# Performance work log

Measured on AMD Instinct MI355X. Metric: run time of the kernel, lower is better.

## Reference

```python
import jax, jax.numpy as jnp
import numpy as np

B, C, H, W = 4, 256, 64, 64
CQK = C // 16  # 16


def conv2d(x, w, b):
    # x: [B,C,H,W], w: [O,I,3,3], SAME padding, stride 1
    y = jax.lax.conv_general_dilated(
        x, w, window_strides=(1, 1), padding='SAME',
        dimension_numbers=('NCHW', 'OIHW', 'NCHW'))
    return y + b[None, :, None, None]


def setup_inputs() -> dict:
    key = jax.random.key(0)
    ks = jax.random.split(key, 8)
    fan_in = C * 9
    s = 1.0 / np.sqrt(fan_in)
    return {
        'x': jax.random.normal(ks[0], (B, C, H, W), jnp.float32),
        'y': jax.random.normal(ks[1], (B, C, H, W), jnp.float32),
        'wq': jax.random.normal(ks[2], (CQK, C, 3, 3), jnp.float32) * s,
        'bq': jnp.zeros((CQK,), jnp.float32),
        'wk': jax.random.normal(ks[3], (CQK, C, 3, 3), jnp.float32) * s,
        'bk': jnp.zeros((CQK,), jnp.float32),
        'wv': jax.random.normal(ks[4], (C, C, 3, 3), jnp.float32) * s,
        'bv': jnp.zeros((C,), jnp.float32),
    }


def reference(x, y, wq, bq, wk, bk, wv, bv):
    b, c, h, w = x.shape
    n = h * w
    q = conv2d(x, wq, bq).reshape(b, -1, n)            # [B,CQK,N]
    k = conv2d(y, wk, bk).reshape(b, -1, n)            # [B,CQK,N]
    v = conv2d(y, wv, bv).reshape(b, c, n)             # [B,C,N]
    # energy[b,i,j] = sum_d q[b,d,i] * k[b,d,j]  (unscaled, as in source)
    energy = jnp.einsum('bdi,bdj->bij', q, k)          # [B,N,N]
    attn = jax.nn.softmax(energy, axis=-1)
    # out[b,c,i] = sum_j v[b,c,j] * attn[b,i,j]
    out = jnp.einsum('bcj,bij->bci', v, attn)
    return out.reshape(b, c, h, w)
```

## Files before the change

### kernel.cpp

```cpp
#include <hip/hip_runtime.h>
#include <stdint.h>


typedef __bf16 bf16;
typedef bf16 bf16x8 __attribute__((ext_vector_type(8)));
typedef float f32x4 __attribute__((ext_vector_type(4)));
typedef unsigned long long ull;

#define DEV static __device__ __forceinline__

DEV f32x4 mfma16(bf16x8 a, bf16x8 b, f32x4 c) {
  return __builtin_amdgcn_mfma_f32_16x16x32_bf16(a, b, c, 0, 0, 0);
}

#define SMBUF 25344
#define YSLAB 4224

__global__ void pack_all_kernel(const float* __restrict__ wv, const float* __restrict__ wq,
                                const float* __restrict__ wk, bf16* __restrict__ W3v,
                                bf16* __restrict__ W3q, bf16* __restrict__ W3k) {
  int idx = blockIdx.x * 256 + threadIdx.x;
  if (idx >= 663552) return;
  const float* src;
  bf16* dst;
  int rel, O;
  if (idx < 589824)      { src = wv; dst = W3v; rel = idx; O = 256; }
  else if (idx < 626688) { src = wq; dst = W3q; rel = idx - 589824; O = 16; }
  else                   { src = wk; dst = W3k; rel = idx - 626688; O = 16; }
  int o = rel / 2304, r = rel - o * 2304;
  int ci = r / 9, tap = r - ci * 9;
  int chunk = ci >> 6, c6 = ci & 63;
  int ks = (tap << 1) + (c6 >> 5), j = c6 & 31;
  dst[((chunk * 18 + ks) * O + o) * 32 + j] = (bf16)src[rel];
}

DEV void stage_load(float4* xv, const float* __restrict__ img, int b, int h, int ci0, int t) {
  const int wg = t & 15, clq = t >> 4;
#pragma unroll
  for (int dh = 0; dh < 3; ++dh) {
    int hh = h + dh - 1;
    bool ok = (hh >= 0) && (hh < 64);
#pragma unroll
    for (int cc = 0; cc < 4; ++cc) {
      float4 v = make_float4(0.f, 0.f, 0.f, 0.f);
      if (ok) v = *(const float4*)&img[((((size_t)b << 8) + ci0 + (clq << 2) + cc) * 64 + hh) * 64 + (wg << 2)];
      xv[dh * 4 + cc] = v;
    }
  }
}

DEV void stage_write(char* smc, const float4* xv, int t) {
  if (t < 96) {
    int dh = t >> 5, r = t & 31;
    int wH = (r & 16) ? 65 : 0, cq = r & 15;
    *(ull*)(smc + ((((dh * 66 + wH) << 7) + (cq << 3)) ^ ((wH & 7) << 4))) = 0ull;
  }
  const int wg = t & 15, clq = t >> 4;
#pragma unroll
  for (int dh = 0; dh < 3; ++dh) {
    const float4 a = xv[dh * 4 + 0], b4 = xv[dh * 4 + 1], c4 = xv[dh * 4 + 2], d4 = xv[dh * 4 + 3];
    const float ax[4] = {a.x, a.y, a.z, a.w};
    const float bx[4] = {b4.x, b4.y, b4.z, b4.w};
    const float cx[4] = {c4.x, c4.y, c4.z, c4.w};
    const float dx[4] = {d4.x, d4.y, d4.z, d4.w};
#pragma unroll
    for (int q4 = 0; q4 < 4; ++q4) {
      int wH = (wg << 2) + q4 + 1;
      union { bf16 h4[4]; ull v; } pk;
      pk.h4[0] = (bf16)ax[q4]; pk.h4[1] = (bf16)bx[q4];
      pk.h4[2] = (bf16)cx[q4]; pk.h4[3] = (bf16)dx[q4];
      *(ull*)(smc + ((((dh * 66 + wH) << 7) + (clq << 3)) ^ ((wH & 7) << 4))) = pk.v;
    }
  }
}

DEV void yF_write(bf16* __restrict__ yFo, const float4* xv, int b, int h, int chunk, int t) {
  const int wg = t & 15, clq = t >> 4;
  const int half = clq >> 3, gr = clq & 7;
  ull* base = (ull*)yFo + ((size_t)(((b * 64 + h) * 4 + chunk) * 2 + half) * 66) * 8 + gr;
  const float4 a = xv[4 + 0], b4 = xv[4 + 1], c4 = xv[4 + 2], d4 = xv[4 + 3];
  const float ax[4] = {a.x, a.y, a.z, a.w};
  const float bx[4] = {b4.x, b4.y, b4.z, b4.w};
  const float cx[4] = {c4.x, c4.y, c4.z, c4.w};
  const float dx[4] = {d4.x, d4.y, d4.z, d4.w};
#pragma unroll
  for (int q4 = 0; q4 < 4; ++q4) {
    int wH = (wg << 2) + q4 + 1;
    union { bf16 h4[4]; ull v; } pk;
    pk.h4[0] = (bf16)ax[q4]; pk.h4[1] = (bf16)bx[q4];
    pk.h4[2] = (bf16)cx[q4]; pk.h4[3] = (bf16)dx[q4];
    base[(size_t)wH * 8] = pk.v;
  }
}

__global__ __launch_bounds__(256) void conv_qk_kernel(
    const float* __restrict__ x, const float* __restrict__ y,
    const bf16* __restrict__ W3q, const bf16* __restrict__ W3k,
    const float* __restrict__ bq, const float* __restrict__ bk,
    bf16* __restrict__ qT, bf16* __restrict__ kT, bf16* __restrict__ yFo) {
  __shared__ __align__(16) char smc[2 * SMBUF];
  const int mode = blockIdx.x >> 8;
  const float* img = mode ? y : x;
  const bf16* W3 = mode ? W3k : W3q;
  const float* bias = mode ? bk : bq;
  const int bi = blockIdx.x & 255;
  const int t = threadIdx.x;
  const int lane = t & 63, wv = t >> 6;
  const int g = lane >> 4, ln = lane & 15;
  const int b = bi >> 6;
  const int h = bi & 63;
  f32x4 acc = {0.f, 0.f, 0.f, 0.f};
  float4 xv[12];
  stage_load(xv, img, b, h, 0, t);
  if (mode) {
    if (t < 128) {
      int chunk = t >> 5, half = (t >> 4) & 1, wside = (t >> 3) & 1, gr = t & 7;
      int wH = wside ? 65 : 0;
      ((ull*)yFo)[((size_t)(((b * 64 + h) * 4 + chunk) * 2 + half) * 66 + wH) * 8 + gr] = 0ull;
    }
    yF_write(yFo, xv, b, h, 0, t);
  }
  stage_write(smc, xv, t);
  __syncthreads();
  for (int chunk = 0; chunk < 4; ++chunk) {
    char* cur = smc + (chunk & 1) * SMBUF;
    if (chunk < 3) {
      stage_load(xv, img, b, h, (chunk + 1) << 6, t);
      if (mode) yF_write(yFo, xv, b, h, chunk + 1, t);
    }
#pragma unroll
    for (int ks = 0; ks < 18; ++ks) {
      const int tap = ks >> 1, clb = (ks & 1) << 5;
      const int kh = tap / 3, kw = tap - kh * 3;
      const int wH = (wv << 4) + ln + kw;
      uint32_t bo = ((((kh * 66 + wH) << 6) + clb + (g << 3)) << 1) ^ ((wH & 7) << 4);
      bf16x8 bfr = *(const bf16x8*)(cur + bo);
      bf16x8 afr = *(const bf16x8*)&W3[(size_t)((chunk * 18 + ks) * 16 + ln) * 32 + (g << 3)];
      acc = mfma16(afr, bfr, acc);
    }
    if (chunk < 3) stage_write(smc + ((chunk + 1) & 1) * SMBUF, xv, t);
    __syncthreads();
  }
  const int p = (h << 6) + (wv << 4) + ln;
#pragma unroll
  for (int r = 0; r < 4; ++r) {
    int o = (g << 2) + r;
    float val = acc[r] + bias[o];
    if (mode == 0) {
      val *= 1.4426950408889634f;
      bf16* drow = qT + (((size_t)b << 12) + p) * 64;
      bf16 hi = (bf16)val;
      drow[o] = hi;
      drow[16 + o] = hi;
      drow[32 + o] = (bf16)(val - (float)hi);
      drow[48 + o] = (bf16)0.f;
    } else {
      bf16* drow = kT + (((size_t)b << 12) + p) * 32;
      bf16 hi = (bf16)val;
      drow[o] = hi;
      drow[16 + o] = (bf16)(val - (float)hi);
    }
  }
}

__global__ __launch_bounds__(256) void conv_v_kernel(
    const bf16* __restrict__ yF, const bf16* __restrict__ W3,
    const float* __restrict__ bias, bf16* __restrict__ VF) {
  __shared__ __align__(16) char smc[6 * YSLAB];
  const int t = threadIdx.x;
  const int lane = t & 63, wv = t >> 6;
  const int g = lane >> 4, ln = lane & 15;
  const int raw = blockIdx.x;
  const int b = raw >> 8;
  const int h = (raw >> 2) & 63;
  const int oh = raw & 3;
  const int obase = (oh << 6) + (wv << 4);
  const int kh0 = (h == 0) ? 1 : 0, kh1 = (h == 63) ? 2 : 3;
  f32x4 acc[4];
#pragma unroll
  for (int wf = 0; wf < 4; ++wf) acc[wf] = (f32x4){0.f, 0.f, 0.f, 0.f};

  f32x4 xmain[6];
  f32x4 xtail[6];
#define YBASE(kh, half, chunk) ((const char*)yF + \
    (size_t)((((b * 64 + (h + (kh) - 1)) * 4 + (chunk)) * 2 + (half)) * YSLAB))

#define LOADC(chunk)                                                       \
  {                                                                        \
    _Pragma("unroll")                                                      \
    for (int kh = 0; kh < 3; ++kh)                                         \
      if (kh >= kh0 && kh < kh1)                                           \
        _Pragma("unroll")                                                  \
        for (int half = 0; half < 2; ++half) {                             \
          const char* src = YBASE(kh, half, chunk);                        \
          xmain[kh * 2 + half] = *(const f32x4*)(src + (t << 4));          \
          if (t < 8) xtail[kh * 2 + half] = *(const f32x4*)(src + 4096 + (t << 4)); \
        }                                                                  \
  }

#define WRITEC()                                                           \
  {                                                                        \
    _Pragma("unroll")                                                      \
    for (int kh = 0; kh < 3; ++kh)                                         \
      if (kh >= kh0 && kh < kh1)                                           \
        _Pragma("unroll")                                                  \
        for (int half = 0; half < 2; ++half) {                             \
          char* dst = smc + (kh * 2 + half) * YSLAB;                       \
          *(f32x4*)(dst + (t << 4)) = xmain[kh * 2 + half];                \
          if (t < 8) *(f32x4*)(dst + 4096 + (t << 4)) = xtail[kh * 2 + half]; \
        }                                                                  \
  }

  LOADC(0)
  WRITEC()
  __syncthreads();
  for (int chunk = 0; chunk < 4; ++chunk) {
    if (chunk < 3) LOADC(chunk + 1)
#pragma unroll
    for (int kh = 0; kh < 3; ++kh) {
      if (kh < kh0 || kh >= kh1) continue;
      bf16x8 afr[6];
#pragma unroll
      for (int i = 0; i < 6; ++i) {
        const int ks = kh * 6 + i;
        afr[i] = *(const bf16x8*)&W3[(size_t)((chunk * 18 + ks) * 256 + obase + ln) * 32 + (g << 3)];
      }
#pragma unroll
      for (int i = 0; i < 6; ++i) {
        const int kw = i >> 1, half = i & 1;
        const char* lrow = smc + (kh * 2 + half) * YSLAB + ((ln + kw) << 6) + (g << 4);
#pragma unroll
        for (int wf = 0; wf < 4; ++wf) {
          bf16x8 bfr = *(const bf16x8*)(lrow + (wf << 10));
          acc[wf] = mfma16(afr[i], bfr, acc[wf]);
        }
      }
    }
    if (chunk < 3) {
      __syncthreads();
      WRITEC()
      __syncthreads();
    }
  }
#undef YBASE
#undef LOADC
#undef WRITEC
  const int cblk = obase >> 4;
#pragma unroll
  for (int r = 0; r < 4; ++r) {
    int c = obase + (g << 2) + r;
    int lnv = c & 15;
    float bvv = bias[c];
#pragma unroll
    for (int wf = 0; wf < 4; ++wf) {
      int p = (h << 6) + (wf << 4) + ln;
      int J = p >> 5, gv = (p >> 3) & 3, e = p & 7;
      VF[(((size_t)(((b << 7) + J) << 4) + cblk) << 9) + (gv << 7) + (lnv << 3) + e] =
          (bf16)(acc[wf][r] + bvv);
    }
  }
}

__global__ __launch_bounds__(512, 2) void attn_kernel(
    const bf16* __restrict__ qT, const bf16* __restrict__ kT,
    const bf16* __restrict__ VF, float* __restrict__ outp) {
  __shared__ __align__(16) char Klds[2 * 4096];
  __shared__ __align__(16) char Plds[2 * 8192];
  __shared__ float lsumS[4][16];
  const int raw = blockIdx.x;
  const int b  = raw & 3;
  const int it = raw >> 2;
  const int i0 = it << 6;
  const int t = threadIdx.x;
  const int lane = t & 63, wv = t >> 6;
  const int g = lane >> 4, ln = lane & 15;
  const bool prod = (wv < 4);
  const int f = wv & 3;
  const int cb = f << 6;
  const int cblk0 = f << 2;

  const char* kTb = (const char*)kT + (((size_t)b << 12) << 6);
  const char* vfb = (const char*)VF + ((size_t)b << 21);

  bf16x8 bq1 = {}, bq2 = {};
  if (prod) {
    const bf16* qrow = &qT[(((size_t)b << 12) + i0 + (f << 4) + ln) * 64];
    bq1 = *(const bf16x8*)&qrow[g << 3];
    bq2 = *(const bf16x8*)&qrow[32 + (g << 3)];
  }
  float lsum = 0.f;
  const int krow = t >> 2, kc = t & 3;
  const uint32_t kwoff = ((uint32_t)krow << 6) + ((uint32_t)(kc ^ (krow & 3)) << 4);

  f32x4 acc[4][4];
#pragma unroll
  for (int cf = 0; cf < 4; ++cf)
#pragma unroll
    for (int ff = 0; ff < 4; ++ff) acc[cf][ff] = (f32x4){0.f, 0.f, 0.f, 0.f};
  bf16x8 avA[8], avB[8];

  if (prod)
    *(f32x4*)(Klds + kwoff) = *(const f32x4*)(kTb + ((size_t)krow << 6) + (kc << 4));
  __syncthreads();

  for (int m = 0; m < 32; ++m) {
    const int jtA = m << 1;
    if (prod) {
      f32x4 s[4];
#pragma unroll
      for (int jf = 0; jf < 4; ++jf) {
        const int row = (jf << 4) + ln;
        bf16x8 ak = *(const bf16x8*)(Klds + ((uint32_t)row << 6) + ((uint32_t)(g ^ (row & 3)) << 4));
        f32x4 z = {0.f, 0.f, 0.f, 0.f};
        s[jf] = mfma16(ak, bq2, mfma16(ak, bq1, z));
      }
#pragma unroll
      for (int jf = 0; jf < 4; ++jf) {
        union { bf16 h[4]; ull v; } pk;
#pragma unroll
        for (int r = 0; r < 4; ++r) {
          float pv = __builtin_amdgcn_exp2f(s[jf][r]);
          lsum += pv;
          pk.h[r] = (bf16)pv;
        }
        uint32_t bo = (((uint32_t)f << 11) + ((uint32_t)ln << 7) + (jf << 5) + (g << 3)) ^ ((ln & 7) << 4);
        *(ull*)(Plds + bo) = pk.v;
      }
      *(f32x4*)(Klds + 4096 + kwoff) =
          *(const f32x4*)(kTb + ((size_t)(((jtA + 1) << 6) + krow) << 6) + (kc << 4));
    } else {
#pragma unroll
      for (int ks = 0; ks < 2; ++ks)
#pragma unroll
        for (int cf = 0; cf < 4; ++cf)
          avB[ks * 4 + cf] = *(const bf16x8*)(vfb +
              ((size_t)(((jtA << 1) + ks) * 16 + cblk0 + cf) << 10) + (lane << 4));
      if (m > 0) {
        __builtin_amdgcn_s_setprio(1);
#pragma unroll
        for (int ks = 0; ks < 2; ++ks) {
          bf16x8 bp[4];
#pragma unroll
          for (int ff = 0; ff < 4; ++ff) {
            uint32_t bo = (8192u + ((uint32_t)ff << 11) + ((uint32_t)ln << 7) + (ks << 6) + (g << 4)) ^ ((ln & 7) << 4);
            bp[ff] = *(const bf16x8*)(Plds + bo);
          }
#pragma unroll
          for (int cf = 0; cf < 4; ++cf)
#pragma unroll
            for (int ff = 0; ff < 4; ++ff)
              acc[cf][ff] = mfma16(avA[ks * 4 + cf], bp[ff], acc[cf][ff]);
        }
        __builtin_amdgcn_s_setprio(0);
      }
    }
    __syncthreads();
    const int jtB = jtA + 1;
    if (prod) {
      f32x4 s[4];
#pragma unroll
      for (int jf = 0; jf < 4; ++jf) {
        const int row = (jf << 4) + ln;
        bf16x8 ak = *(const bf16x8*)(Klds + 4096 + ((uint32_t)row << 6) + ((uint32_t)(g ^ (row & 3)) << 4));
        f32x4 z = {0.f, 0.f, 0.f, 0.f};
        s[jf] = mfma16(ak, bq2, mfma16(ak, bq1, z));
      }
#pragma unroll
      for (int jf = 0; jf < 4; ++jf) {
        union { bf16 h[4]; ull v; } pk;
#pragma unroll
        for (int r = 0; r < 4; ++r) {
          float pv = __builtin_amdgcn_exp2f(s[jf][r]);
          lsum += pv;
          pk.h[r] = (bf16)pv;
        }
        uint32_t bo = (8192u + ((uint32_t)f << 11) + ((uint32_t)ln << 7) + (jf << 5) + (g << 3)) ^ ((ln & 7) << 4);
        *(ull*)(Plds + bo) = pk.v;
      }
      if (m < 31)
        *(f32x4*)(Klds + kwoff) =
            *(const f32x4*)(kTb + ((size_t)(((jtB + 1) << 6) + krow) << 6) + (kc << 4));
    } else {
#pragma unroll
      for (int ks = 0; ks < 2; ++ks)
#pragma unroll
        for (int cf = 0; cf < 4; ++cf)
          avA[ks * 4 + cf] = *(const bf16x8*)(vfb +
              ((size_t)(((jtB << 1) + ks) * 16 + cblk0 + cf) << 10) + (lane << 4));
      __builtin_amdgcn_s_setprio(1);
#pragma unroll
      for (int ks = 0; ks < 2; ++ks) {
        bf16x8 bp[4];
#pragma unroll
        for (int ff = 0; ff < 4; ++ff) {
          uint32_t bo = (((uint32_t)ff << 11) + ((uint32_t)ln << 7) + (ks << 6) + (g << 4)) ^ ((ln & 7) << 4);
          bp[ff] = *(const bf16x8*)(Plds + bo);
        }
#pragma unroll
        for (int cf = 0; cf < 4; ++cf)
#pragma unroll
          for (int ff = 0; ff < 4; ++ff)
            acc[cf][ff] = mfma16(avB[ks * 4 + cf], bp[ff], acc[cf][ff]);
      }
      __builtin_amdgcn_s_setprio(0);
    }
    __syncthreads();
  }
  if (prod) {
    float l = lsum;
    l += __shfl_xor(l, 16, 64);
    l += __shfl_xor(l, 32, 64);
    if (g == 0) lsumS[f][ln] = l;
  } else {
#pragma unroll
    for (int ks = 0; ks < 2; ++ks) {
      bf16x8 bp[4];
#pragma unroll
      for (int ff = 0; ff < 4; ++ff) {
        uint32_t bo = (8192u + ((uint32_t)ff << 11) + ((uint32_t)ln << 7) + (ks << 6) + (g << 4)) ^ ((ln & 7) << 4);
        bp[ff] = *(const bf16x8*)(Plds + bo);
      }
#pragma unroll
      for (int cf = 0; cf < 4; ++cf)
#pragma unroll
        for (int ff = 0; ff < 4; ++ff)
          acc[cf][ff] = mfma16(avA[ks * 4 + cf], bp[ff], acc[cf][ff]);
    }
  }
  __syncthreads();
  if (!prod) {
#pragma unroll
    for (int ff = 0; ff < 4; ++ff) {
      float rdiv = 1.f / lsumS[ff][ln];
      const int i = i0 + (ff << 4) + ln;
#pragma unroll
      for (int cf = 0; cf < 4; ++cf)
#pragma unroll
        for (int r = 0; r < 4; ++r) {
          int c = cb + (cf << 4) + (g << 2) + r;
          outp[(((size_t)b << 8) + c) * 4096 + i] = acc[cf][ff][r] * rdiv;
        }
    }
  }
}

extern "C" void kernel_launch(void* const* d_in, const int* in_sizes, int n_in,
                              void* d_out, int out_size, void* d_ws, size_t ws_size,
                              hipStream_t stream) {
  const float* x  = (const float*)d_in[0];
  const float* y  = (const float*)d_in[1];
  const float* wq = (const float*)d_in[2];
  const float* bq = (const float*)d_in[3];
  const float* wk = (const float*)d_in[4];
  const float* bk = (const float*)d_in[5];
  const float* wv = (const float*)d_in[6];
  const float* bv = (const float*)d_in[7];
  float* out = (float*)d_out;

  char* ws = (char*)d_ws;
  bf16* qT  = (bf16*)(ws);
  bf16* kT  = (bf16*)(ws + (2u << 20));
  bf16* VF  = (bf16*)(ws + (3u << 20));
  bf16* W3v = (bf16*)(ws + (11u << 20));
  bf16* W3q = (bf16*)(ws + (11u << 20) + 1179648u);
  bf16* W3k = (bf16*)(ws + (11u << 20) + 1179648u + 73728u);
  bf16* yF  = (bf16*)(ws + (13u << 20));

  pack_all_kernel<<<2592, 256, 0, stream>>>(wv, wq, wk, W3v, W3q, W3k);
  conv_qk_kernel<<<512, 256, 0, stream>>>(x, y, W3q, W3k, bq, bk, qT, kT, yF);
  conv_v_kernel<<<1024, 256, 0, stream>>>(yF, W3v, bv, VF);
  attn_kernel<<<256, 512, 0, stream>>>(qT, kT, VF, out);
}
```

Baseline: 118.1 us.

## Double KV tile width per barrier step in producer/consumer attention loop

```diff
diff --git a/kernel.cpp b/kernel.cpp
--- a/kernel.cpp
+++ b/kernel.cpp
@@ -264,8 +264,8 @@
 __global__ __launch_bounds__(512, 2) void attn_kernel(
     const bf16* __restrict__ qT, const bf16* __restrict__ kT,
     const bf16* __restrict__ VF, float* __restrict__ outp) {
-  __shared__ __align__(16) char Klds[2 * 4096];
-  __shared__ __align__(16) char Plds[2 * 8192];
+  __shared__ __align__(16) char Klds[2 * 8192];
+  __shared__ __align__(16) char Plds[2 * 16384];
   __shared__ float lsumS[4][16];
   const int raw = blockIdx.x;
   const int b  = raw & 3;
@@ -289,120 +289,88 @@
     bq2 = *(const bf16x8*)&qrow[32 + (g << 3)];
   }
   float lsum = 0.f;
-  const int krow = t >> 2, kc = t & 3;
-  const uint32_t kwoff = ((uint32_t)krow << 6) + ((uint32_t)(kc ^ (krow & 3)) << 4);
+  const int row0 = t >> 1, kc0 = ((t & 1) << 1);
+  const int kc1 = kc0 + 1;
+  const uint32_t kwA = ((uint32_t)row0 << 6) + ((uint32_t)(kc0 ^ (row0 & 3)) << 4);
+  const uint32_t kwB = ((uint32_t)row0 << 6) + ((uint32_t)(kc1 ^ (row0 & 3)) << 4);
 
   f32x4 acc[4][4];
 #pragma unroll
   for (int cf = 0; cf < 4; ++cf)
 #pragma unroll
     for (int ff = 0; ff < 4; ++ff) acc[cf][ff] = (f32x4){0.f, 0.f, 0.f, 0.f};
-  bf16x8 avA[8], avB[8];
-
-  if (prod)
-    *(f32x4*)(Klds + kwoff) = *(const f32x4*)(kTb + ((size_t)krow << 6) + (kc << 4));
+  bf16x8 avX[8], avY[8];
+
+#define KSTAGE(TILE, KB)                                                          \
+  {                                                                               \
+    const char* ksrc = kTb + (size_t)(((TILE) << 7) + row0) * 64;                 \
+    f32x4 kv0 = *(const f32x4*)(ksrc + (kc0 << 4));                               \
+    f32x4 kv1 = *(const f32x4*)(ksrc + (kc1 << 4));                               \
+    *(f32x4*)(Klds + (KB) + kwA) = kv0;                                           \
+    *(f32x4*)(Klds + (KB) + kwB) = kv1;                                           \
+  }
+
+#define CONS_LOAD(AV, TILE, H)                                                    \
+  {                                                                               \
+    _Pragma("unroll")                                                             \
+    for (int ks2 = 0; ks2 < 2; ++ks2)                                             \
+      _Pragma("unroll")                                                           \
+      for (int cf = 0; cf < 4; ++cf)                                              \
+        AV[ks2 * 4 + cf] = *(const bf16x8*)(vfb +                                 \
+            ((size_t)((((TILE) << 2) + ((H) << 1) + ks2) * 16 + cblk0 + cf) << 10) + (lane << 4)); \
+  }
+
+#define CONS_PV(AV, PB, H)                                                        \
+  {                                                                               \
+    __builtin_amdgcn_s_setprio(1);                                                \
+    _Pragma("unroll")                                                             \
+    for (int ks2 = 0; ks2 < 2; ++ks2) {                                           \
+      bf16x8 bp[4];                                                               \
+      _Pragma("unroll")                                                           \
+      for (int ff = 0; ff < 4; ++ff) {                                            \
+        uint32_t bo = ((PB) + ((uint32_t)ff << 12) + ((uint32_t)ln << 8) +        \
+                       ((((H) << 1) + ks2) << 6) + (g << 4)) ^ ((ln & 7) << 4);   \
+        bp[ff] = *(const bf16x8*)(Plds + bo);                                     \
+      }                                                                           \
+      _Pragma("unroll")                                                           \
+      for (int cf = 0; cf < 4; ++cf)                                              \
+        _Pragma("unroll")                                                         \
+        for (int ff = 0; ff < 4; ++ff)                                            \
+          acc[cf][ff] = mfma16(AV[ks2 * 4 + cf], bp[ff], acc[cf][ff]);            \
+    }                                                                             \
+    __builtin_amdgcn_s_setprio(0);                                                \
+  }
+
+  if (prod) KSTAGE(0, 0u)
   __syncthreads();
 
   for (int m = 0; m < 32; ++m) {
-    const int jtA = m << 1;
+    const uint32_t kb  = (uint32_t)(m & 1) << 13;
+    const uint32_t pbw = (uint32_t)(m & 1) << 14;
+    const uint32_t pbr = (uint32_t)((m + 1) & 1) << 14;
     if (prod) {
-      f32x4 s[4];
-#pragma unroll
-      for (int jf = 0; jf < 4; ++jf) {
+#pragma unroll
+      for (int jf = 0; jf < 8; ++jf) {
         const int row = (jf << 4) + ln;
-        bf16x8 ak = *(const bf16x8*)(Klds + ((uint32_t)row << 6) + ((uint32_t)(g ^ (row & 3)) << 4));
+        bf16x8 ak = *(const bf16x8*)(Klds + kb + ((uint32_t)row << 6) + ((uint32_t)(g ^ (row & 3)) << 4));
         f32x4 z = {0.f, 0.f, 0.f, 0.f};
-        s[jf] = mfma16(ak, bq2, mfma16(ak, bq1, z));
-      }
-#pragma unroll
-      for (int jf = 0; jf < 4; ++jf) {
-        union { bf16 h[4]; ull v; } pk;
+        f32x4 s = mfma16(ak, bq2, mfma16(ak, bq1, z));
+        union { bf16 h4[4]; ull v; } pk;
 #pragma unroll
         for (int r = 0; r < 4; ++r) {
-          float pv = __builtin_amdgcn_exp2f(s[jf][r]);
+          float pv = __builtin_amdgcn_exp2f(s[r]);
           lsum += pv;
-          pk.h[r] = (bf16)pv;
+          pk.h4[r] = (bf16)pv;
         }
-        uint32_t bo = (((uint32_t)f << 11) + ((uint32_t)ln << 7) + (jf << 5) + (g << 3)) ^ ((ln & 7) << 4);
+        uint32_t bo = (pbw + ((uint32_t)f << 12) + ((uint32_t)ln << 8) + (jf << 5) + (g << 3)) ^ ((ln & 7) << 4);
         *(ull*)(Plds + bo) = pk.v;
       }
-      *(f32x4*)(Klds + 4096 + kwoff) =
-          *(const f32x4*)(kTb + ((size_t)(((jtA + 1) << 6) + krow) << 6) + (kc << 4));
+      if (m < 31) KSTAGE(m + 1, kb ^ 8192u)
     } else {
-#pragma unroll
-      for (int ks = 0; ks < 2; ++ks)
-#pragma unroll
-        for (int cf = 0; cf < 4; ++cf)
-          avB[ks * 4 + cf] = *(const bf16x8*)(vfb +
-              ((size_t)(((jtA << 1) + ks) * 16 + cblk0 + cf) << 10) + (lane << 4));
-      if (m > 0) {
-        __builtin_amdgcn_s_setprio(1);
-#pragma unroll
-        for (int ks = 0; ks < 2; ++ks) {
-          bf16x8 bp[4];
-#pragma unroll
-          for (int ff = 0; ff < 4; ++ff) {
-            uint32_t bo = (8192u + ((uint32_t)ff << 11) + ((uint32_t)ln << 7) + (ks << 6) + (g << 4)) ^ ((ln & 7) << 4);
-            bp[ff] = *(const bf16x8*)(Plds + bo);
-          }
-#pragma unroll
-          for (int cf = 0; cf < 4; ++cf)
-#pragma unroll
-            for (int ff = 0; ff < 4; ++ff)
-              acc[cf][ff] = mfma16(avA[ks * 4 + cf], bp[ff], acc[cf][ff]);
-        }
-        __builtin_amdgcn_s_setprio(0);
-      }
-    }
-    __syncthreads();
-    const int jtB = jtA + 1;
-    if (prod) {
-      f32x4 s[4];
-#pragma unroll
-      for (int jf = 0; jf < 4; ++jf) {
-        const int row = (jf << 4) + ln;
-        bf16x8 ak = *(const bf16x8*)(Klds + 4096 + ((uint32_t)row << 6) + ((uint32_t)(g ^ (row & 3)) << 4));
-        f32x4 z = {0.f, 0.f, 0.f, 0.f};
-        s[jf] = mfma16(ak, bq2, mfma16(ak, bq1, z));
-      }
-#pragma unroll
-      for (int jf = 0; jf < 4; ++jf) {
-        union { bf16 h[4]; ull v; } pk;
-#pragma unroll
-        for (int r = 0; r < 4; ++r) {
-          float pv = __builtin_amdgcn_exp2f(s[jf][r]);
-          lsum += pv;
-          pk.h[r] = (bf16)pv;
-        }
-        uint32_t bo = (8192u + ((uint32_t)f << 11) + ((uint32_t)ln << 7) + (jf << 5) + (g << 3)) ^ ((ln & 7) << 4);
-        *(ull*)(Plds + bo) = pk.v;
-      }
-      if (m < 31)
-        *(f32x4*)(Klds + kwoff) =
-            *(const f32x4*)(kTb + ((size_t)(((jtB + 1) << 6) + krow) << 6) + (kc << 4));
-    } else {
-#pragma unroll
-      for (int ks = 0; ks < 2; ++ks)
-#pragma unroll
-        for (int cf = 0; cf < 4; ++cf)
-          avA[ks * 4 + cf] = *(const bf16x8*)(vfb +
-              ((size_t)(((jtB << 1) + ks) * 16 + cblk0 + cf) << 10) + (lane << 4));
-      __builtin_amdgcn_s_setprio(1);
-#pragma unroll
-      for (int ks = 0; ks < 2; ++ks) {
-        bf16x8 bp[4];
-#pragma unroll
-        for (int ff = 0; ff < 4; ++ff) {
-          uint32_t bo = (((uint32_t)ff << 11) + ((uint32_t)ln << 7) + (ks << 6) + (g << 4)) ^ ((ln & 7) << 4);
-          bp[ff] = *(const bf16x8*)(Plds + bo);
-        }
-#pragma unroll
-        for (int cf = 0; cf < 4; ++cf)
-#pragma unroll
-          for (int ff = 0; ff < 4; ++ff)
-            acc[cf][ff] = mfma16(avB[ks * 4 + cf], bp[ff], acc[cf][ff]);
-      }
-      __builtin_amdgcn_s_setprio(0);
+      if (m > 0) CONS_PV(avX, pbr, 0)
+      CONS_LOAD(avX, m, 0)
+      if (m > 0) CONS_PV(avY, pbr, 1)
+      CONS_LOAD(avY, m, 1)
     }
     __syncthreads();
   }
@@ -412,20 +380,8 @@
     l += __shfl_xor(l, 32, 64);
     if (g == 0) lsumS[f][ln] = l;
   } else {
-#pragma unroll
-    for (int ks = 0; ks < 2; ++ks) {
-      bf16x8 bp[4];
-#pragma unroll
-      for (int ff = 0; ff < 4; ++ff) {
-        uint32_t bo = (8192u + ((uint32_t)ff << 11) + ((uint32_t)ln << 7) + (ks << 6) + (g << 4)) ^ ((ln & 7) << 4);
-        bp[ff] = *(const bf16x8*)(Plds + bo);
-      }
-#pragma unroll
-      for (int cf = 0; cf < 4; ++cf)
-#pragma unroll
-        for (int ff = 0; ff < 4; ++ff)
-          acc[cf][ff] = mfma16(avA[ks * 4 + cf], bp[ff], acc[cf][ff]);
-    }
+    CONS_PV(avX, 16384u, 0)
+    CONS_PV(avY, 16384u, 1)
   }
   __syncthreads();
   if (!prod) {
@@ -442,6 +398,9 @@
         }
     }
   }
+#undef KSTAGE
+#undef CONS_LOAD
+#undef CONS_PV
 }
 
 extern "C" void kernel_launch(void* const* d_in, const int* in_sizes, int n_in,
```

New measurement: 122.6 us. 3.8% more time.
